# Kernel tuning notes

Measured on AMD Instinct MI355X. Metric: run time of the kernel, lower is better.

Reference implementation:

```python
import jax, jax.numpy as jnp
import numpy as np

DIM = 512
HIDDEN = 1024
NUM_EXPERTS = 8
TOP_K = 2
BALANCE_LOSS_WEIGHT = 0.01


def setup_inputs() -> dict:
    key = jax.random.key(0)
    ks = jax.random.split(key, 6)
    B, S = 4, 8192
    x = jax.random.normal(ks[0], (B, S, DIM), dtype=jnp.float32)
    # Linear params (stored already transposed for x @ W convenience)
    scale_in = 1.0 / np.sqrt(DIM)
    scale_hid = 1.0 / np.sqrt(HIDDEN)
    gate_w = jax.random.uniform(ks[1], (DIM, NUM_EXPERTS), jnp.float32, -scale_in, scale_in)
    w1 = jax.random.uniform(ks[2], (NUM_EXPERTS, DIM, HIDDEN), jnp.float32, -scale_in, scale_in)
    b1 = jax.random.uniform(ks[3], (NUM_EXPERTS, HIDDEN), jnp.float32, -scale_in, scale_in)
    w2 = jax.random.uniform(ks[4], (NUM_EXPERTS, HIDDEN, DIM), jnp.float32, -scale_hid, scale_hid)
    b2 = jax.random.uniform(ks[5], (NUM_EXPERTS, DIM), jnp.float32, -scale_hid, scale_hid)
    return {"x": x, "gate_w": gate_w, "w1": w1, "b1": b1, "w2": w2, "b2": b2}


def reference(x, gate_w, w1, b1, w2, b2):
    B, S, D = x.shape
    T = B * S
    E = gate_w.shape[1]
    flat_x = x.reshape(T, D)

    # Gating (eval mode: no noise)
    gate_logits = flat_x @ gate_w                      # [T, E]
    gates = jax.nn.softmax(gate_logits, axis=-1)
    top_k_gates, top_k_indices = jax.lax.top_k(gates, TOP_K)
    top_k_gates = top_k_gates / jnp.sum(top_k_gates, axis=-1, keepdims=True)

    rows = jnp.arange(T)[:, None]
    # Per-token combine weight for each expert (0 if not selected)
    combine_w = jnp.zeros((T, E), flat_x.dtype).at[rows, top_k_indices].add(top_k_gates)
    # Load-balance loss (indices are discrete -> constant mask)
    expert_mask = jnp.zeros((T, E), flat_x.dtype).at[rows, top_k_indices].set(1.0)
    expert_usage = expert_mask.sum(0) / T
    balance_loss = jnp.mean((expert_usage - 1.0 / E) ** 2) * E * BALANCE_LOSS_WEIGHT

    # Expert MLPs; unselected tokens have combine weight 0 so contribute nothing,
    # matching the original masked gather/scatter math exactly.
    out = jnp.zeros_like(flat_x)
    for e in range(E):  # small fixed expert count
        h = jax.nn.gelu(flat_x @ w1[e] + b1[e], approximate=False)  # [T, HIDDEN]
        out = out + (h @ w2[e] + b2[e]) * combine_w[:, e:e + 1]
    return out.reshape(B, S, D), balance_loss
```

## Files before the change

### kernel.cpp

```cpp
#include <hip/hip_runtime.h>
#include <stdint.h>

#define T_TOK 32768
#define DDIM 512
#define HID 1024
#define NEXP 8

typedef _Float16 f16;
typedef _Float16 f16x8 __attribute__((ext_vector_type(8)));
typedef _Float16 f16x4 __attribute__((ext_vector_type(4)));
typedef float f32x4 __attribute__((ext_vector_type(4)));

__device__ __forceinline__ void gload_lds16(const void* g, void* l) {
  __builtin_amdgcn_global_load_lds(
      (__attribute__((address_space(1))) void*)g,
      (__attribute__((address_space(3))) void*)l, 16, 0, 0);
}

__global__ void k_cvt_x(const float* __restrict__ x, f16* __restrict__ xh) {
  int i = blockIdx.x * blockDim.x + threadIdx.x;
  float4 v = ((const float4*)x)[i];
  f16x4 o = {(f16)v.x, (f16)v.y, (f16)v.z, (f16)v.w};
  ((f16x4*)xh)[i] = o;
}

__global__ void k_transpose(const float* __restrict__ W, f16* __restrict__ Wt,
                            const int K, const int N) {
  __shared__ float tile[64][65];
  const int e = blockIdx.z;
  const float* Wb = W + (size_t)e * K * N;
  f16* Wtb = Wt + (size_t)e * K * N;
  const int k0 = blockIdx.x * 64, n0 = blockIdx.y * 64;
  const int tr = threadIdx.x >> 2;
  const int tc = (threadIdx.x & 3) * 16;
#pragma unroll
  for (int j = 0; j < 16; j += 4) {
    float4 v = *(const float4*)&Wb[(size_t)(k0 + tr) * N + n0 + tc + j];
    tile[tr][tc + j + 0] = v.x; tile[tr][tc + j + 1] = v.y;
    tile[tr][tc + j + 2] = v.z; tile[tr][tc + j + 3] = v.w;
  }
  __syncthreads();
  f16x8 t0, t1;
#pragma unroll
  for (int j = 0; j < 8; ++j) {
    t0[j] = (f16)tile[tc + j][tr];
    t1[j] = (f16)tile[tc + 8 + j][tr];
  }
  *(f16x8*)&Wtb[(size_t)(n0 + tr) * K + k0 + tc] = t0;
  *(f16x8*)&Wtb[(size_t)(n0 + tr) * K + k0 + tc + 8] = t1;
}

__global__ void k_gate(const float* __restrict__ x, const float* __restrict__ gw,
                       int* __restrict__ route_e, float* __restrict__ route_w,
                       int* __restrict__ cnt) {
  __shared__ int scnt[NEXP];
  const int tid = threadIdx.x, lane = tid & 63, wv = tid >> 6;
  if (tid < NEXP) scnt[tid] = 0;
  __syncthreads();

  float ga[4][8], gb[4][8];
#pragma unroll
  for (int j = 0; j < 4; ++j) {
    const int r0 = lane * 4 + j;
    const int r1 = 256 + lane * 4 + j;
    float4 q0 = *(const float4*)&gw[r0 * 8];
    float4 q1 = *(const float4*)&gw[r0 * 8 + 4];
    ga[j][0] = q0.x; ga[j][1] = q0.y; ga[j][2] = q0.z; ga[j][3] = q0.w;
    ga[j][4] = q1.x; ga[j][5] = q1.y; ga[j][6] = q1.z; ga[j][7] = q1.w;
    q0 = *(const float4*)&gw[r1 * 8];
    q1 = *(const float4*)&gw[r1 * 8 + 4];
    gb[j][0] = q0.x; gb[j][1] = q0.y; gb[j][2] = q0.z; gb[j][3] = q0.w;
    gb[j][4] = q1.x; gb[j][5] = q1.y; gb[j][6] = q1.z; gb[j][7] = q1.w;
  }

  const int tbase = blockIdx.x * 32 + wv * 8;
  for (int it = 0; it < 8; ++it) {
    const int t = tbase + it;
    const float4 A = *(const float4*)&x[(size_t)t * DDIM + lane * 4];
    const float4 B = *(const float4*)&x[(size_t)t * DDIM + 256 + lane * 4];
    float p[8];
#pragma unroll
    for (int e = 0; e < 8; ++e) {
      p[e] = A.x * ga[0][e] + A.y * ga[1][e] + A.z * ga[2][e] + A.w * ga[3][e] +
             B.x * gb[0][e] + B.y * gb[1][e] + B.z * gb[2][e] + B.w * gb[3][e];
    }
#pragma unroll
    for (int off = 32; off >= 1; off >>= 1) {
#pragma unroll
      for (int e = 0; e < 8; ++e) p[e] += __shfl_xor(p[e], off);
    }
    if (lane == 0) {
      int e1 = 0;
#pragma unroll
      for (int e = 1; e < 8; ++e) if (p[e] > p[e1]) e1 = e;
      int e2 = (e1 == 0) ? 1 : 0;
#pragma unroll
      for (int e = 0; e < 8; ++e) if (e != e1 && p[e] > p[e2]) e2 = e;
      const float wa = 1.0f / (1.0f + expf(p[e2] - p[e1]));
      route_e[t] = e1 | (e2 << 8);
      route_w[t] = wa;
      atomicAdd(&scnt[e1], 1);
      atomicAdd(&scnt[e2], 1);
    }
  }
  __syncthreads();
  if (tid < NEXP) atomicAdd(&cnt[tid], scnt[tid]);
}

__global__ void k_scan(const int* __restrict__ cnt, int* __restrict__ base,
                       int* __restrict__ cursor, float* __restrict__ out_loss) {
  if (threadIdx.x == 0) {
    int b = 0;
    float loss = 0.0f;
    for (int e = 0; e < NEXP; ++e) {
      base[e] = b;
      cursor[e] = b;
      b += cnt[e];
      float u = (float)cnt[e] / (float)T_TOK - 0.125f;
      loss += u * u;
    }
    *out_loss = loss * 0.01f;
  }
}

__global__ void k_scatter(const int* __restrict__ route_e, const float* __restrict__ route_w,
                          int* __restrict__ cursor, int* __restrict__ tok_slot,
                          float* __restrict__ wgt_slot) {
  const int t = blockIdx.x * blockDim.x + threadIdx.x;
  const int lane = threadIdx.x & 63;
  const int re = route_e[t];
  const float wa = route_w[t];
  const int e1 = re & 0xff, e2 = re >> 8;
#pragma unroll
  for (int e = 0; e < NEXP; ++e) {
    unsigned long long m = __ballot(e1 == e);
    if (m) {
      const int leader = __ffsll(m) - 1;
      int b0 = 0;
      if (lane == leader) b0 = atomicAdd(&cursor[e], __popcll(m));
      b0 = __shfl(b0, leader);
      if (e1 == e) {
        const int pos = b0 + __popcll(m & ((1ull << lane) - 1));
        tok_slot[pos] = t;
        wgt_slot[pos] = wa;
      }
    }
    m = __ballot(e2 == e);
    if (m) {
      const int leader = __ffsll(m) - 1;
      int b0 = 0;
      if (lane == leader) b0 = atomicAdd(&cursor[e], __popcll(m));
      b0 = __shfl(b0, leader);
      if (e2 == e) {
        const int pos = b0 + __popcll(m & ((1ull << lane) - 1));
        tok_slot[pos] = t;
        wgt_slot[pos] = 1.0f - wa;
      }
    }
  }
}

__global__ __launch_bounds__(256) void k_mlp1(
    const f16* __restrict__ xh, const f16* __restrict__ w1t,
    const float* __restrict__ b1, f16* __restrict__ h,
    const int* __restrict__ tok_slot, const int* __restrict__ base,
    const int* __restrict__ cnt, const int hc, const int c0) {
  const int e = blockIdx.z;
  const int ne = cnt[e];
  const int m0 = blockIdx.x * 128;
  if (m0 >= ne) return;
  const int n0 = blockIdx.y * 128;
  const int sbase = base[e];
  const int slot0 = sbase + m0;
  const int shi = sbase + ne;

  __shared__ f16 As[128 * 64];
  __shared__ f16 Bs[128 * 64];

  const int tid = threadIdx.x;
  const int lane = tid & 63;
  const int wv = tid >> 6;
  const int wm = wv >> 1, wn = wv & 1;
  const int g = lane >> 4;
  const int l15 = lane & 15;

  const f16* aSrc[4];
  const f16* bSrc[4];
#pragma unroll
  for (int i = 0; i < 4; ++i) {
    const int ch = wv * 4 + i;
    const int row = ch * 8 + (lane >> 3);
    const int p = lane & 7;
    const int sw = (p ^ (row & 7)) * 8;
    int slot = slot0 + row;
    slot = (slot <= shi - 1) ? slot : (shi - 1);
    const int tok = tok_slot[slot];
    aSrc[i] = xh + (size_t)tok * DDIM + sw;
    bSrc[i] = w1t + (size_t)(e * HID + c0 + n0 + row) * DDIM + sw;
  }

  f32x4 acc[4][4];
#pragma unroll
  for (int a = 0; a < 4; ++a)
#pragma unroll
    for (int b = 0; b < 4; ++b) { f32x4 z = {0.f, 0.f, 0.f, 0.f}; acc[a][b] = z; }

  for (int ks = 0; ks < DDIM / 64; ++ks) {
    const int k0 = ks * 64;
#pragma unroll
    for (int i = 0; i < 4; ++i) {
      gload_lds16(aSrc[i] + k0, &As[(wv * 4 + i) * 512]);
      gload_lds16(bSrc[i] + k0, &Bs[(wv * 4 + i) * 512]);
    }
    __syncthreads();
#pragma unroll
    for (int kb = 0; kb < 2; ++kb) {
      f16x8 af[4], bf[4];
#pragma unroll
      for (int mf = 0; mf < 4; ++mf) {
        const int row = wm * 64 + mf * 16 + l15;
        af[mf] = *(const f16x8*)&As[row * 64 + (((kb * 4 + g) ^ (row & 7)) * 8)];
      }
#pragma unroll
      for (int nf = 0; nf < 4; ++nf) {
        const int row = wn * 64 + nf * 16 + l15;
        bf[nf] = *(const f16x8*)&Bs[row * 64 + (((kb * 4 + g) ^ (row & 7)) * 8)];
      }
#pragma unroll
      for (int mf = 0; mf < 4; ++mf)
#pragma unroll
        for (int nf = 0; nf < 4; ++nf)
          acc[mf][nf] = __builtin_amdgcn_mfma_f32_16x16x32_f16(af[mf], bf[nf], acc[mf][nf], 0, 0, 0);
    }
    __syncthreads();
  }

#pragma unroll
  for (int mf = 0; mf < 4; ++mf) {
#pragma unroll
    for (int r = 0; r < 4; ++r) {
      const int row = wm * 64 + mf * 16 + g * 4 + r;
      const int slot = slot0 + row;
      if (slot >= shi) continue;
#pragma unroll
      for (int nf = 0; nf < 4; ++nf) {
        const int col = wn * 64 + nf * 16 + l15;
        float v = acc[mf][nf][r] + b1[e * HID + c0 + n0 + col];
        v = 0.5f * v * (1.0f + erff(v * 0.70710678118654752f));
        h[(size_t)slot * hc + n0 + col] = (f16)v;
      }
    }
  }
}

__global__ __launch_bounds__(256) void k_mlp2(
    const f16* __restrict__ h, const f16* __restrict__ w2t,
    const float* __restrict__ b2, float* __restrict__ out,
    const int* __restrict__ tok_slot, const float* __restrict__ wgt_slot,
    const int* __restrict__ base, const int* __restrict__ cnt,
    const int hc, const int c0) {
  const int e = blockIdx.z;
  const int ne = cnt[e];
  const int m0 = blockIdx.x * 128;
  if (m0 >= ne) return;
  const int n0 = blockIdx.y * 128;
  const int sbase = base[e];
  const int slot0 = sbase + m0;
  const int shi = sbase + ne;

  __shared__ f16 As[128 * 64];
  __shared__ f16 Bs[128 * 64];

  const int tid = threadIdx.x;
  const int lane = tid & 63;
  const int wv = tid >> 6;
  const int wm = wv >> 1, wn = wv & 1;
  const int g = lane >> 4;
  const int l15 = lane & 15;

  const f16* aSrc[4];
  const f16* bSrc[4];
#pragma unroll
  for (int i = 0; i < 4; ++i) {
    const int ch = wv * 4 + i;
    const int row = ch * 8 + (lane >> 3);
    const int p = lane & 7;
    const int sw = (p ^ (row & 7)) * 8;
    int slot = slot0 + row;
    slot = (slot <= 2 * T_TOK - 1) ? slot : (2 * T_TOK - 1);
    aSrc[i] = h + (size_t)slot * hc + sw;
    bSrc[i] = w2t + (size_t)(e * DDIM + n0 + row) * HID + c0 + sw;
  }

  f32x4 acc[4][4];
#pragma unroll
  for (int a = 0; a < 4; ++a)
#pragma unroll
    for (int b = 0; b < 4; ++b) { f32x4 z = {0.f, 0.f, 0.f, 0.f}; acc[a][b] = z; }

  for (int ks = 0; ks < hc / 64; ++ks) {
    const int k0 = ks * 64;
#pragma unroll
    for (int i = 0; i < 4; ++i) {
      gload_lds16(aSrc[i] + k0, &As[(wv * 4 + i) * 512]);
      gload_lds16(bSrc[i] + k0, &Bs[(wv * 4 + i) * 512]);
    }
    __syncthreads();
#pragma unroll
    for (int kb = 0; kb < 2; ++kb) {
      f16x8 af[4], bf[4];
#pragma unroll
      for (int mf = 0; mf < 4; ++mf) {
        const int row = wm * 64 + mf * 16 + l15;
        af[mf] = *(const f16x8*)&As[row * 64 + (((kb * 4 + g) ^ (row & 7)) * 8)];
      }
#pragma unroll
      for (int nf = 0; nf < 4; ++nf) {
        const int row = wn * 64 + nf * 16 + l15;
        bf[nf] = *(const f16x8*)&Bs[row * 64 + (((kb * 4 + g) ^ (row & 7)) * 8)];
      }
#pragma unroll
      for (int mf = 0; mf < 4; ++mf)
#pragma unroll
        for (int nf = 0; nf < 4; ++nf)
          acc[mf][nf] = __builtin_amdgcn_mfma_f32_16x16x32_f16(af[mf], bf[nf], acc[mf][nf], 0, 0, 0);
    }
    __syncthreads();
  }

#pragma unroll
  for (int mf = 0; mf < 4; ++mf) {
#pragma unroll
    for (int r = 0; r < 4; ++r) {
      const int row = wm * 64 + mf * 16 + g * 4 + r;
      const int slot = slot0 + row;
      if (slot >= shi) continue;
      const int tok = tok_slot[slot];
      const float w = wgt_slot[slot];
      float* orow = out + (size_t)tok * DDIM + n0;
#pragma unroll
      for (int nf = 0; nf < 4; ++nf) {
        const int col = wn * 64 + nf * 16 + l15;
        float v = acc[mf][nf][r];
        if (c0 == 0) v += b2[e * DDIM + n0 + col];
        unsafeAtomicAdd(orow + col, w * v);
      }
    }
  }
}

extern "C" void kernel_launch(void* const* d_in, const int* in_sizes, int n_in,
                              void* d_out, int out_size, void* d_ws, size_t ws_size,
                              hipStream_t stream) {
  (void)in_sizes; (void)n_in;
  const float* x  = (const float*)d_in[0];
  const float* gw = (const float*)d_in[1];
  const float* w1 = (const float*)d_in[2];
  const float* b1 = (const float*)d_in[3];
  const float* w2 = (const float*)d_in[4];
  const float* b2 = (const float*)d_in[5];
  float* out = (float*)d_out;

  char* ws = (char*)d_ws;
  size_t off = 0;
  auto alloc = [&](size_t bytes) {
    char* p = ws + off;
    off += (bytes + 255) & ~(size_t)255;
    return p;
  };
  f16*   xh       = (f16*)  alloc((size_t)T_TOK * DDIM * 2);
  f16*   w1t      = (f16*)  alloc((size_t)NEXP * DDIM * HID * 2);
  f16*   w2t      = (f16*)  alloc((size_t)NEXP * DDIM * HID * 2);
  int*   route_e  = (int*)  alloc((size_t)T_TOK * 4);
  float* route_w  = (float*)alloc((size_t)T_TOK * 4);
  int*   tok_slot = (int*)  alloc((size_t)2 * T_TOK * 4);
  float* wgt_slot = (float*)alloc((size_t)2 * T_TOK * 4);
  int*   cnt      = (int*)  alloc(256);
  int*   base     = cnt + 8;
  int*   cursor   = cnt + 16;
  f16*   hbuf     = (f16*)(ws + off);
  const size_t havail = (ws_size > off) ? (ws_size - off) : 0;

  int ns = 8;
  const int cands[4] = {1, 2, 4, 8};
  for (int i = 0; i < 4; ++i) {
    if ((size_t)2 * T_TOK * (HID / cands[i]) * 2 <= havail) { ns = cands[i]; break; }
  }
  const int hc = HID / ns;

  hipMemsetAsync(cnt, 0, 32, stream);
  hipMemsetAsync(d_out, 0, (size_t)out_size * sizeof(float), stream);

  k_cvt_x<<<dim3(T_TOK * DDIM / 4 / 256), 256, 0, stream>>>(x, xh);
  k_transpose<<<dim3(DDIM / 64, HID / 64, NEXP), 256, 0, stream>>>(w1, w1t, DDIM, HID);
  k_transpose<<<dim3(HID / 64, DDIM / 64, NEXP), 256, 0, stream>>>(w2, w2t, HID, DDIM);
  k_gate<<<dim3(T_TOK / 32), 256, 0, stream>>>(x, gw, route_e, route_w, cnt);
  k_scan<<<1, 64, 0, stream>>>(cnt, base, cursor, out + (size_t)T_TOK * DDIM);
  k_scatter<<<dim3(T_TOK / 256), 256, 0, stream>>>(route_e, route_w, cursor, tok_slot, wgt_slot);

  for (int c = 0; c < ns; ++c) {
    k_mlp1<<<dim3(256, hc / 128, NEXP), 256, 0, stream>>>(
        xh, w1t, b1, hbuf, tok_slot, base, cnt, hc, c * hc);
    k_mlp2<<<dim3(256, DDIM / 128, NEXP), 256, 0, stream>>>(
        hbuf, w2t, b2, out, tok_slot, wgt_slot, base, cnt, hc, c * hc);
  }
}
```

Measured before the change: 704.0 us.

## Double-buffer LDS tiles in both expert GEMM kernels to overlap loads with MFMA

Both expert MLP GEMM kernels now keep two LDS buffer pairs and alternate between them. The next K-tile is issued with global_load_lds before the MFMA work on the current tile, and one barrier per tile replaces two. The aim is to hide global-to-LDS load latency behind matrix math. The cost is doubling LDS per block to 64KB, which can lower how many blocks fit on a CU. The loop also assumes an even tile count.

```diff
diff --git a/kernel.cpp b/kernel.cpp
--- a/kernel.cpp
+++ b/kernel.cpp
@@ -159,6 +159,33 @@
     }
   }
 }
+
+#define STAGE_TILE(k0_, As_, Bs_)                                   \
+  do {                                                              \
+    _Pragma("unroll") for (int i = 0; i < 4; ++i) {                 \
+      gload_lds16(aSrc[i] + (k0_), &(As_)[(wv * 4 + i) * 512]);     \
+      gload_lds16(bSrc[i] + (k0_), &(Bs_)[(wv * 4 + i) * 512]);     \
+    }                                                               \
+  } while (0)
+
+#define COMPUTE_TILE(As_, Bs_)                                                    \
+  do {                                                                            \
+    _Pragma("unroll") for (int kb = 0; kb < 2; ++kb) {                            \
+      f16x8 af[4], bf[4];                                                         \
+      _Pragma("unroll") for (int mf = 0; mf < 4; ++mf) {                          \
+        const int row = wm * 64 + mf * 16 + l15;                                  \
+        af[mf] = *(const f16x8*)&(As_)[row * 64 + (((kb * 4 + g) ^ (row & 7)) * 8)]; \
+      }                                                                           \
+      _Pragma("unroll") for (int nf = 0; nf < 4; ++nf) {                          \
+        const int row = wn * 64 + nf * 16 + l15;                                  \
+        bf[nf] = *(const f16x8*)&(Bs_)[row * 64 + (((kb * 4 + g) ^ (row & 7)) * 8)]; \
+      }                                                                           \
+      _Pragma("unroll") for (int mf = 0; mf < 4; ++mf)                            \
+        _Pragma("unroll") for (int nf = 0; nf < 4; ++nf)                          \
+          acc[mf][nf] =                                                           \
+              __builtin_amdgcn_mfma_f32_16x16x32_f16(af[mf], bf[nf], acc[mf][nf], 0, 0, 0); \
+    }                                                                             \
+  } while (0)
 
 __global__ __launch_bounds__(256) void k_mlp1(
     const f16* __restrict__ xh, const f16* __restrict__ w1t,
@@ -174,8 +201,10 @@
   const int slot0 = sbase + m0;
   const int shi = sbase + ne;
 
-  __shared__ f16 As[128 * 64];
-  __shared__ f16 Bs[128 * 64];
+  __shared__ f16 As0[128 * 64];
+  __shared__ f16 Bs0[128 * 64];
+  __shared__ f16 As1[128 * 64];
+  __shared__ f16 Bs1[128 * 64];
 
   const int tid = threadIdx.x;
   const int lane = tid & 63;
@@ -205,33 +234,15 @@
 #pragma unroll
     for (int b = 0; b < 4; ++b) { f32x4 z = {0.f, 0.f, 0.f, 0.f}; acc[a][b] = z; }
 
-  for (int ks = 0; ks < DDIM / 64; ++ks) {
-    const int k0 = ks * 64;
-#pragma unroll
-    for (int i = 0; i < 4; ++i) {
-      gload_lds16(aSrc[i] + k0, &As[(wv * 4 + i) * 512]);
-      gload_lds16(bSrc[i] + k0, &Bs[(wv * 4 + i) * 512]);
-    }
+  const int NT = DDIM / 64;
+  STAGE_TILE(0, As0, Bs0);
+  __syncthreads();
+  for (int t = 0; t < NT; t += 2) {
+    if (t + 1 < NT) STAGE_TILE((t + 1) * 64, As1, Bs1);
+    COMPUTE_TILE(As0, Bs0);
     __syncthreads();
-#pragma unroll
-    for (int kb = 0; kb < 2; ++kb) {
-      f16x8 af[4], bf[4];
-#pragma unroll
-      for (int mf = 0; mf < 4; ++mf) {
-        const int row = wm * 64 + mf * 16 + l15;
-        af[mf] = *(const f16x8*)&As[row * 64 + (((kb * 4 + g) ^ (row & 7)) * 8)];
-      }
-#pragma unroll
-      for (int nf = 0; nf < 4; ++nf) {
-        const int row = wn * 64 + nf * 16 + l15;
-        bf[nf] = *(const f16x8*)&Bs[row * 64 + (((kb * 4 + g) ^ (row & 7)) * 8)];
-      }
-#pragma unroll
-      for (int mf = 0; mf < 4; ++mf)
-#pragma unroll
-        for (int nf = 0; nf < 4; ++nf)
-          acc[mf][nf] = __builtin_amdgcn_mfma_f32_16x16x32_f16(af[mf], bf[nf], acc[mf][nf], 0, 0, 0);
-    }
+    if (t + 2 < NT) STAGE_TILE((t + 2) * 64, As0, Bs0);
+    COMPUTE_TILE(As1, Bs1);
     __syncthreads();
   }
 
@@ -268,8 +279,10 @@
   const int slot0 = sbase + m0;
   const int shi = sbase + ne;
 
-  __shared__ f16 As[128 * 64];
-  __shared__ f16 Bs[128 * 64];
+  __shared__ f16 As0[128 * 64];
+  __shared__ f16 Bs0[128 * 64];
+  __shared__ f16 As1[128 * 64];
+  __shared__ f16 Bs1[128 * 64];
 
   const int tid = threadIdx.x;
   const int lane = tid & 63;
@@ -298,33 +311,15 @@
 #pragma unroll
     for (int b = 0; b < 4; ++b) { f32x4 z = {0.f, 0.f, 0.f, 0.f}; acc[a][b] = z; }
 
-  for (int ks = 0; ks < hc / 64; ++ks) {
-    const int k0 = ks * 64;
-#pragma unroll
-    for (int i = 0; i < 4; ++i) {
-      gload_lds16(aSrc[i] + k0, &As[(wv * 4 + i) * 512]);
-      gload_lds16(bSrc[i] + k0, &Bs[(wv * 4 + i) * 512]);
-    }
+  const int NT = hc / 64;
+  STAGE_TILE(0, As0, Bs0);
+  __syncthreads();
+  for (int t = 0; t < NT; t += 2) {
+    if (t + 1 < NT) STAGE_TILE((t + 1) * 64, As1, Bs1);
+    COMPUTE_TILE(As0, Bs0);
     __syncthreads();
-#pragma unroll
-    for (int kb = 0; kb < 2; ++kb) {
-      f16x8 af[4], bf[4];
-#pragma unroll
-      for (int mf = 0; mf < 4; ++mf) {
-        const int row = wm * 64 + mf * 16 + l15;
-        af[mf] = *(const f16x8*)&As[row * 64 + (((kb * 4 + g) ^ (row & 7)) * 8)];
-      }
-#pragma unroll
-      for (int nf = 0; nf < 4; ++nf) {
-        const int row = wn * 64 + nf * 16 + l15;
-        bf[nf] = *(const f16x8*)&Bs[row * 64 + (((kb * 4 + g) ^ (row & 7)) * 8)];
-      }
-#pragma unroll
-      for (int mf = 0; mf < 4; ++mf)
-#pragma unroll
-        for (int nf = 0; nf < 4; ++nf)
-          acc[mf][nf] = __builtin_amdgcn_mfma_f32_16x16x32_f16(af[mf], bf[nf], acc[mf][nf], 0, 0, 0);
-    }
+    if (t + 2 < NT) STAGE_TILE((t + 2) * 64, As0, Bs0);
+    COMPUTE_TILE(As1, Bs1);
     __syncthreads();
   }
 
```

After: 655.9 us. 1.07x faster.
